# Kernel tuning notes

Hardware: AMD Instinct MI355X
Metric: run time of the kernel (lower is better)

The kernel has to match this reference:

```python
import jax, jax.numpy as jnp
import numpy as np

B, N, DIM, H, DH = 2, 2048, 256, 8, 32
DIM_INNER = H * DH  # 256


def setup_inputs() -> dict:
    key = jax.random.key(0)
    ks = jax.random.split(key, 8)
    s = DIM ** -0.5  # keep activations / logits in a sane range
    return {
        "x_real": jax.random.normal(ks[0], (B, N, DIM), jnp.float32),
        "x_imag": jax.random.normal(ks[1], (B, N, DIM), jnp.float32),
        "wq_r": jax.random.normal(ks[2], (DIM, DIM_INNER), jnp.float32) * s,
        "wq_i": jax.random.normal(ks[3], (DIM, DIM_INNER), jnp.float32) * s,
        "wkv_r": jax.random.normal(ks[4], (DIM, 2 * DIM_INNER), jnp.float32) * s,
        "wkv_i": jax.random.normal(ks[5], (DIM, 2 * DIM_INNER), jnp.float32) * s,
        "wo_r": jax.random.normal(ks[6], (DIM_INNER, DIM), jnp.float32) * s,
        "wo_i": jax.random.normal(ks[7], (DIM_INNER, DIM), jnp.float32) * s,
    }


def _clin(xr, xi, wr, wi):
    # complex linear: (xr + i xi) @ (wr + i wi)
    return xr @ wr - xi @ wi, xr @ wi + xi @ wr


def _split_heads(t):
    b, n, _ = t.shape
    return t.reshape(b, n, H, DH).transpose(0, 2, 1, 3)  # b h n d


def _merge_heads(t):
    b, h, n, d = t.shape
    return t.transpose(0, 2, 1, 3).reshape(b, n, h * d)


def reference(x_real, x_imag, wq_r, wq_i, wkv_r, wkv_i, wo_r, wo_i):
    # complex projections
    qr, qi = _clin(x_real, x_imag, wq_r, wq_i)
    kvr, kvi = _clin(x_real, x_imag, wkv_r, wkv_i)
    kr, vr = jnp.split(kvr, 2, axis=-1)
    ki, vi = jnp.split(kvi, 2, axis=-1)
    qr, qi, kr, ki, vr, vi = map(_split_heads, (qr, qi, kr, ki, vr, vi))

    # complex_attention_complete (sec 3.2 eq 3): 4 real SDPA replicas.
    # q repeat '(c r b)' -> blocks [qr, qr, qi, qi]; k repeat '(r c b)' -> [kr, ki, kr, ki]
    scale = DH ** -0.5
    Q = jnp.stack([qr, qr, qi, qi])        # [4, b, h, n, d]
    K = jnp.stack([kr, ki, kr, ki])
    sim = jnp.einsum('rbhid,rbhjd->rbhij', Q, K) * scale
    A = jax.nn.softmax(sim, axis=-1)       # [4, b, h, n, n]

    av = lambda a, v: jnp.einsum('bhij,bhjd->bhid', a, v)
    # sign-recombine trick: indices [0,3,5,6 | 1,2,4,7], sign [[1,-1,-1,-1],[1,1,1,-1]]
    o_r = av(A[0], vr) - av(A[1], vi) - av(A[2], vi) - av(A[3], vr)
    o_i = av(A[0], vi) + av(A[1], vr) + av(A[2], vr) - av(A[3], vi)

    mr, mi = _merge_heads(o_r), _merge_heads(o_i)
    out_r, out_i = _clin(mr, mi, wo_r, wo_i)
    # real view of the complex output: [b, n, dim, 2]
    return jnp.stack([out_r, out_i], axis=-1)
```

## Files before the change

### kernel.cpp

```cpp
#include <hip/hip_runtime.h>
#include <hip/hip_bf16.h>
#include <math.h>

namespace {
constexpr int kB = 2, kN = 2048, kDim = 256, kH = 8, kDH = 32;
constexpr int kBH = kB * kH;
constexpr long kPlane = (long)kBH * kN * kDH;
constexpr float kQScaleL2 = 0.25506852552f;
}

typedef unsigned short u16;
typedef short short8 __attribute__((ext_vector_type(8)));
typedef short short4v __attribute__((ext_vector_type(4)));
typedef float floatx16 __attribute__((ext_vector_type(16)));
#define MFMA_BF16(a, b, c) __builtin_amdgcn_mfma_f32_32x32x16_bf16(a, b, c, 0, 0, 0)

__device__ inline u16 bf16b(float x) {
    union { float f; unsigned u; } c; c.f = x;
    unsigned r = c.u + 0x7FFFu + ((c.u >> 16) & 1u);
    return (u16)(r >> 16);
}
__device__ inline unsigned pack2(float x, float y) {
    return (unsigned)bf16b(x) | ((unsigned)bf16b(y) << 16);
}
__device__ inline unsigned packtr(float lo, float hi) {
    return __builtin_amdgcn_perm(__float_as_uint(hi), __float_as_uint(lo), 0x07060302u);
}
__device__ inline short8 mk8(const float* e) {
    union { unsigned u[4]; short8 s; } c;
    c.u[0] = packtr(e[0], e[1]);
    c.u[1] = packtr(e[2], e[3]);
    c.u[2] = packtr(e[4], e[5]);
    c.u[3] = packtr(e[6], e[7]);
    return c.s;
}

__global__ __launch_bounds__(256, 2) void prep_w(
    const float* __restrict__ wq_r, const float* __restrict__ wq_i,
    const float* __restrict__ wkv_r, const float* __restrict__ wkv_i,
    const float* __restrict__ wo_r, const float* __restrict__ wo_i,
    u16* __restrict__ Wbig, u16* __restrict__ WoT)
{
    const long base = ((long)blockIdx.x * 256 + threadIdx.x) * 4;
    if (base < 786432) {
        const int c = (int)(base >> 9);
        const int k = (int)(base & 511);
        const int g = c >> 8, d = c & 255;
        const bool hi = k >= 256;
        const int k2 = hi ? k - 256 : k;
        const float* src;
        float sgn = 1.f;
        int col, stride;
        if (g < 2) {
            stride = 256; col = d;
            if (g == 0) { src = hi ? wq_i : wq_r; if (hi) sgn = -1.f; }
            else        { src = hi ? wq_r : wq_i; }
            sgn *= kQScaleL2;
        } else {
            stride = 512;
            col = (g >= 4) ? d + 256 : d;
            if ((g & 1) == 0) { src = hi ? wkv_i : wkv_r; if (hi) sgn = -1.f; }
            else              { src = hi ? wkv_r : wkv_i; }
        }
        short4v v;
        #pragma unroll
        for (int j = 0; j < 4; ++j)
            v[j] = (short)bf16b(src[(long)(k2 + j) * stride + col] * sgn);
        *(short4v*)(Wbig + base) = v;
    } else {
        const long o = base - 786432;
        const int c = (int)(o >> 9);
        const int k = (int)(o & 511);
        const bool hi = k >= 256;
        const int k2 = hi ? k - 256 : k;
        const float* src;
        float sgn = 1.f;
        int col;
        if (c < 256) { col = c;       src = hi ? wo_i : wo_r; if (hi) sgn = -1.f; }
        else         { col = c - 256; src = hi ? wo_r : wo_i; }
        short4v v;
        #pragma unroll
        for (int j = 0; j < 4; ++j)
            v[j] = (short)bf16b(src[(long)(k2 + j) * 256 + col] * sgn);
        *(short4v*)(WoT + o) = v;
    }
}

__global__ __launch_bounds__(256, 2) void gemm_proj(
    const float* __restrict__ xr_g, const float* __restrict__ xi_g,
    const u16* __restrict__ BT,
    u16* __restrict__ qr, u16* __restrict__ qi, u16* __restrict__ kr,
    u16* __restrict__ ki, u16* __restrict__ vrT, u16* __restrict__ viT)
{
    __shared__ __align__(16) u16 sA[128 * 32];
    __shared__ __align__(16) u16 sB[128 * 32];
    const int tid = threadIdx.x;
    const int lane = tid & 63, l31 = lane & 31, lh = lane >> 5;
    const int w = tid >> 6, wrow = w & 1, wcol = w >> 1;
    const int srow = tid >> 2, sseg = tid & 3;
    const int n0 = blockIdx.x * 128, m0 = blockIdx.y * 128;

    floatx16 a00 = {0}, a01 = {0}, a10 = {0}, a11 = {0};

    for (int kt = 0; kt < 512; kt += 32) {
        __syncthreads();
        const float* xbase = (kt < 256) ? xr_g : xi_g;
        const int kc = (kt & 255) + sseg * 8;
        #pragma unroll
        for (int i = 0; i < 2; ++i) {
            const int r = srow + i * 64;
            {
                const float* src = xbase + (long)(m0 + r) * 256 + kc;
                const float4 f0 = *(const float4*)(src);
                const float4 f1 = *(const float4*)(src + 4);
                union { __hip_bfloat162 b[4]; short8 s; } cv;
                cv.b[0] = __float22bfloat162_rn(make_float2(f0.x, f0.y));
                cv.b[1] = __float22bfloat162_rn(make_float2(f0.z, f0.w));
                cv.b[2] = __float22bfloat162_rn(make_float2(f1.x, f1.y));
                cv.b[3] = __float22bfloat162_rn(make_float2(f1.z, f1.w));
                *(short8*)(sA + r * 32 + sseg * 8) = cv.s;
            }
            *(short8*)(sB + r * 32 + sseg * 8) =
                *(const short8*)(BT + (long)(n0 + r) * 512 + kt + sseg * 8);
        }
        __syncthreads();
        #pragma unroll
        for (int s = 0; s < 2; ++s) {
            const int ko = s * 16 + lh * 8;
            const short8 fa0 = *(const short8*)(sA + (wrow * 64 + l31) * 32 + ko);
            const short8 fa1 = *(const short8*)(sA + (wrow * 64 + 32 + l31) * 32 + ko);
            const short8 fb0 = *(const short8*)(sB + (wcol * 64 + l31) * 32 + ko);
            const short8 fb1 = *(const short8*)(sB + (wcol * 64 + 32 + l31) * 32 + ko);
            a00 = MFMA_BF16(fa0, fb0, a00);
            a01 = MFMA_BF16(fa0, fb1, a01);
            a10 = MFMA_BF16(fa1, fb0, a10);
            a11 = MFMA_BF16(fa1, fb1, a11);
        }
    }

    floatx16 accs[2][2] = {{a00, a01}, {a10, a11}};
    #pragma unroll
    for (int rt = 0; rt < 2; ++rt) {
        #pragma unroll
        for (int ct = 0; ct < 2; ++ct) {
            const int colb = n0 + wcol * 64 + ct * 32;
            const int g = colb >> 8;
            const int h = (colb & 255) >> 5;
            if (g < 4) {
                u16* pl = (g == 0) ? qr : (g == 1) ? qi : (g == 2) ? kr : ki;
                #pragma unroll
                for (int reg = 0; reg < 16; ++reg) {
                    const int row = m0 + wrow * 64 + rt * 32 + (reg & 3) + 8 * (reg >> 2) + 4 * lh;
                    const int b = row >> 11, nn = row & 2047;
                    pl[(((long)(b * 8 + h)) * 2048 + nn) * 32 + l31] = bf16b(accs[rt][ct][reg]);
                }
            } else {
                u16* pl = (g == 4) ? vrT : viT;
                #pragma unroll
                for (int reg = 0; reg < 16; ++reg) {
                    const int row = m0 + wrow * 64 + rt * 32 + (reg & 3) + 8 * (reg >> 2) + 4 * lh;
                    const int b = row >> 11, nn = row & 2047;
                    const int np = (nn & ~12) | ((nn & 4) << 1) | ((nn & 8) >> 1);
                    pl[(((long)(b * 8 + h)) * 32 + l31) * 2048 + np] = bf16b(accs[rt][ct][reg]);
                }
            }
        }
    }
}

__global__ __launch_bounds__(512, 2) void attn_kernel(
    const u16* __restrict__ qr_g, const u16* __restrict__ qi_g,
    const u16* __restrict__ kr_g, const u16* __restrict__ ki_g,
    const u16* __restrict__ vrT_g, const u16* __restrict__ viT_g,
    u16* __restrict__ xo)
{
    __shared__ __align__(16) u16 smem[2][2][2][64 * 40];

    const int tid = threadIdx.x;
    const int lane = tid & 63, l31 = lane & 31, lh = lane >> 5;
    const int w = tid >> 6;
    const int strip = w & 1, qtype = (w >> 1) & 1, jhalf = w >> 2;
    const int bh = blockIdx.x;
    const int i0 = blockIdx.y * 64;
    const long base = (long)bh * kN * kDH;

    const u16* qg = (qtype ? qi_g : qr_g) + base;
    short8 qB0, qB1;
    {
        const u16* qp = qg + (long)(i0 + strip * 32 + l31) * kDH;
        qB0 = *(const short8*)(qp + lh * 8);
        qB1 = *(const short8*)(qp + 16 + lh * 8);
    }

    const int t256 = tid & 255;
    const int srow = t256 & 63;
    const int sseg = t256 >> 6;
    const int t0 = jhalf * 32;
    const u16* kptr = ((srow < 32) ? kr_g : ki_g) + base
                    + ((long)t0 * 32 + (srow & 31)) * kDH + sseg * 8;
    const u16* vptr = ((srow < 32) ? vrT_g : viT_g)
                    + ((long)bh * 32 + (srow & 31)) * kN + (long)t0 * 32 + sseg * 8;

    short8 kreg = *(const short8*)kptr;
    short8 vreg = *(const short8*)vptr;

    floatx16 U0r = {0}, U0i = {0}, U1r = {0}, U1i = {0};
    float la0a = 0.f, la0b = 0.f, la1a = 0.f, la1b = 0.f;

    for (int tt = 0; tt < 32; ++tt) {
        u16* bK = smem[jhalf][0][tt & 1];
        u16* bV = smem[jhalf][1][tt & 1];
        *(short8*)(bK + srow * 40 + sseg * 8) = kreg;
        *(short8*)(bV + srow * 40 + sseg * 8) = vreg;
        __syncthreads();
        if (tt < 31) {
            kreg = *(const short8*)(kptr + (long)(tt + 1) * 1024);
            vreg = *(const short8*)(vptr + (tt + 1) * 32);
        }

        const short8 ka0 = *(const short8*)(bK + l31 * 40 + lh * 8);
        const short8 ka1 = *(const short8*)(bK + l31 * 40 + 16 + lh * 8);
        const short8 kb0 = *(const short8*)(bK + (32 + l31) * 40 + lh * 8);
        const short8 kb1 = *(const short8*)(bK + (32 + l31) * 40 + 16 + lh * 8);
        floatx16 S0 = {0}, S1 = {0};
        S0 = MFMA_BF16(ka0, qB0, S0);
        S0 = MFMA_BF16(ka1, qB1, S0);
        S1 = MFMA_BF16(kb0, qB0, S1);
        S1 = MFMA_BF16(kb1, qB1, S1);

        float e0[16], e1[16];
        #pragma unroll
        for (int r = 0; r < 16; ++r) {
            e0[r] = __builtin_amdgcn_exp2f(S0[r]);
            if (r & 1) la0a += e0[r]; else la0b += e0[r];
        }
        #pragma unroll
        for (int r = 0; r < 16; ++r) {
            e1[r] = __builtin_amdgcn_exp2f(S1[r]);
            if (r & 1) la1a += e1[r]; else la1b += e1[r];
        }
        const short8 F0a = mk8(&e0[0]);
        const short8 F0b = mk8(&e0[8]);
        const short8 F1a = mk8(&e1[0]);
        const short8 F1b = mk8(&e1[8]);

        const short8 va0 = *(const short8*)(bV + l31 * 40 + lh * 8);
        const short8 va1 = *(const short8*)(bV + l31 * 40 + 16 + lh * 8);
        const short8 vb0 = *(const short8*)(bV + (32 + l31) * 40 + lh * 8);
        const short8 vb1 = *(const short8*)(bV + (32 + l31) * 40 + 16 + lh * 8);

        U0r = MFMA_BF16(va0, F0a, U0r);
        U0r = MFMA_BF16(va1, F0b, U0r);
        U0i = MFMA_BF16(vb0, F0a, U0i);
        U0i = MFMA_BF16(vb1, F0b, U0i);
        U1r = MFMA_BF16(va0, F1a, U1r);
        U1r = MFMA_BF16(va1, F1b, U1r);
        U1i = MFMA_BF16(vb0, F1a, U1i);
        U1i = MFMA_BF16(vb1, F1b, U1i);
    }

    float La0 = la0a + la0b;
    float La1 = la1a + la1b;
    La0 += __shfl_xor(La0, 32);
    La1 += __shfl_xor(La1, 32);

    __syncthreads();
    float* sLa = (float*)smem;
    float* sPo = (float*)((u16*)smem + 2048);
    sLa[(w * 2 + 0) * 64 + lane] = La0;
    sLa[(w * 2 + 1) * 64 + lane] = La1;
    __syncthreads();
    const int pw = w ^ 4;
    const float iL0 = 1.f / (La0 + sLa[(pw * 2 + 0) * 64 + lane]);
    const float iL1 = 1.f / (La1 + sLa[(pw * 2 + 1) * 64 + lane]);

    float po_r[16], po_i[16];
    #pragma unroll
    for (int r = 0; r < 16; ++r) {
        if (qtype == 0) {
            po_r[r] =  U0r[r] * iL0 - U1i[r] * iL1;
            po_i[r] =  U0i[r] * iL0 + U1r[r] * iL1;
        } else {
            po_r[r] = -U0i[r] * iL0 - U1r[r] * iL1;
            po_i[r] =  U0r[r] * iL0 - U1i[r] * iL1;
        }
    }

    if (jhalf == 1) {
        float* dst = sPo + ((size_t)(w - 4) * 64 + lane) * 33;
        #pragma unroll
        for (int g = 0; g < 4; ++g) {
            *(float4*)(dst + 4 * g) =
                make_float4(po_r[4 * g], po_r[4 * g + 1], po_r[4 * g + 2], po_r[4 * g + 3]);
            *(float4*)(dst + 16 + 4 * g) =
                make_float4(po_i[4 * g], po_i[4 * g + 1], po_i[4 * g + 2], po_i[4 * g + 3]);
        }
    }
    __syncthreads();
    if (jhalf == 0) {
        const float* src = sPo + ((size_t)w * 64 + lane) * 33;
        #pragma unroll
        for (int g = 0; g < 4; ++g) {
            const float4 ar = *(const float4*)(src + 4 * g);
            const float4 ai = *(const float4*)(src + 16 + 4 * g);
            po_r[4 * g + 0] += ar.x; po_r[4 * g + 1] += ar.y;
            po_r[4 * g + 2] += ar.z; po_r[4 * g + 3] += ar.w;
            po_i[4 * g + 0] += ai.x; po_i[4 * g + 1] += ai.y;
            po_i[4 * g + 2] += ai.z; po_i[4 * g + 3] += ai.w;
        }
    }
    __syncthreads();
    if (jhalf == 0 && qtype == 1) {
        float* dst = sPo + ((size_t)(w - 2) * 64 + lane) * 33;
        #pragma unroll
        for (int g = 0; g < 4; ++g) {
            *(float4*)(dst + 4 * g) =
                make_float4(po_r[4 * g], po_r[4 * g + 1], po_r[4 * g + 2], po_r[4 * g + 3]);
            *(float4*)(dst + 16 + 4 * g) =
                make_float4(po_i[4 * g], po_i[4 * g + 1], po_i[4 * g + 2], po_i[4 * g + 3]);
        }
    }
    __syncthreads();
    if (w < 2) {
        const float* src = sPo + ((size_t)w * 64 + lane) * 33;
        #pragma unroll
        for (int g = 0; g < 4; ++g) {
            const float4 ar = *(const float4*)(src + 4 * g);
            const float4 ai = *(const float4*)(src + 16 + 4 * g);
            po_r[4 * g + 0] += ar.x; po_r[4 * g + 1] += ar.y;
            po_r[4 * g + 2] += ar.z; po_r[4 * g + 3] += ar.w;
            po_i[4 * g + 0] += ai.x; po_i[4 * g + 1] += ai.y;
            po_i[4 * g + 2] += ai.z; po_i[4 * g + 3] += ai.w;
        }
        const int b = bh >> 3, h = bh & 7;
        u16* xrow = xo + ((long)(b * 2048) + i0 + strip * 32 + l31) * 512 + h * 32;
        #pragma unroll
        for (int g = 0; g < 4; ++g) {
            const int d0 = 8 * g + 4 * lh;
            union { unsigned u[2]; uint2 v; } pr, pi;
            pr.u[0] = pack2(po_r[4 * g + 0], po_r[4 * g + 1]);
            pr.u[1] = pack2(po_r[4 * g + 2], po_r[4 * g + 3]);
            pi.u[0] = pack2(po_i[4 * g + 0], po_i[4 * g + 1]);
            pi.u[1] = pack2(po_i[4 * g + 2], po_i[4 * g + 3]);
            *(uint2*)(xrow + d0) = pr.v;
            *(uint2*)(xrow + 256 + d0) = pi.v;
        }
    }
}

__global__ __launch_bounds__(256, 2) void gemm_oproj(
    const u16* __restrict__ Xo, const u16* __restrict__ BT, float* __restrict__ out)
{
    __shared__ __align__(16) u16 sA[128 * 32];
    __shared__ __align__(16) u16 sB[128 * 32];
    const int tid = threadIdx.x;
    const int lane = tid & 63, l31 = lane & 31, lh = lane >> 5;
    const int w = tid >> 6, wrow = w & 1, wcol = w >> 1;
    const int srow = tid >> 2, sseg = tid & 3;
    const int n0 = blockIdx.x * 128, m0 = blockIdx.y * 128;

    floatx16 a00 = {0}, a01 = {0}, a10 = {0}, a11 = {0};

    for (int kt = 0; kt < 512; kt += 32) {
        __syncthreads();
        #pragma unroll
        for (int i = 0; i < 2; ++i) {
            const int r = srow + i * 64;
            *(short8*)(sA + r * 32 + sseg * 8) =
                *(const short8*)(Xo + (long)(m0 + r) * 512 + kt + sseg * 8);
            *(short8*)(sB + r * 32 + sseg * 8) =
                *(const short8*)(BT + (long)(n0 + r) * 512 + kt + sseg * 8);
        }
        __syncthreads();
        #pragma unroll
        for (int s = 0; s < 2; ++s) {
            const int ko = s * 16 + lh * 8;
            const short8 fa0 = *(const short8*)(sA + (wrow * 64 + l31) * 32 + ko);
            const short8 fa1 = *(const short8*)(sA + (wrow * 64 + 32 + l31) * 32 + ko);
            const short8 fb0 = *(const short8*)(sB + (wcol * 64 + l31) * 32 + ko);
            const short8 fb1 = *(const short8*)(sB + (wcol * 64 + 32 + l31) * 32 + ko);
            a00 = MFMA_BF16(fa0, fb0, a00);
            a01 = MFMA_BF16(fa0, fb1, a01);
            a10 = MFMA_BF16(fa1, fb0, a10);
            a11 = MFMA_BF16(fa1, fb1, a11);
        }
    }

    floatx16 accs[2][2] = {{a00, a01}, {a10, a11}};
    #pragma unroll
    for (int rt = 0; rt < 2; ++rt) {
        #pragma unroll
        for (int ct = 0; ct < 2; ++ct) {
            const int colb = n0 + wcol * 64 + ct * 32;
            #pragma unroll
            for (int reg = 0; reg < 16; ++reg) {
                const int row = m0 + wrow * 64 + rt * 32 + (reg & 3) + 8 * (reg >> 2) + 4 * lh;
                const int col = colb + l31;
                const float val = accs[rt][ct][reg];
                if (colb < 256) out[(long)row * 512 + col * 2] = val;
                else            out[(long)row * 512 + (col - 256) * 2 + 1] = val;
            }
        }
    }
}

extern "C" void kernel_launch(void* const* d_in, const int* in_sizes, int n_in,
                              void* d_out, int out_size, void* d_ws, size_t ws_size,
                              hipStream_t stream) {
    const float* xr    = (const float*)d_in[0];
    const float* xi    = (const float*)d_in[1];
    const float* wq_r  = (const float*)d_in[2];
    const float* wq_i  = (const float*)d_in[3];
    const float* wkv_r = (const float*)d_in[4];
    const float* wkv_i = (const float*)d_in[5];
    const float* wo_r  = (const float*)d_in[6];
    const float* wo_i  = (const float*)d_in[7];
    float* out = (float*)d_out;

    u16* ws16 = (u16*)d_ws;
    u16* qr   = ws16 + 0 * kPlane;
    u16* qi   = ws16 + 1 * kPlane;
    u16* kr   = ws16 + 2 * kPlane;
    u16* ki   = ws16 + 3 * kPlane;
    u16* vrT  = ws16 + 4 * kPlane;
    u16* viT  = ws16 + 5 * kPlane;
    u16* xo   = ws16 + 6 * kPlane;
    u16* Wbig = ws16 + 8 * kPlane;
    u16* WoT  = Wbig + 786432;

    prep_w<<<1024, 256, 0, stream>>>(wq_r, wq_i, wkv_r, wkv_i, wo_r, wo_i, Wbig, WoT);
    gemm_proj<<<dim3(12, 32), 256, 0, stream>>>(xr, xi, Wbig, qr, qi, kr, ki, vrT, viT);
    attn_kernel<<<dim3(kBH, kN / 64), 512, 0, stream>>>(qr, qi, kr, ki, vrT, viT, xo);
    gemm_oproj<<<dim3(4, 32), 256, 0, stream>>>(xo, WoT, out);
}
```

Before: 177.8 us.

## Split attention warps by key type instead of key-sequence half

Warps were each assigned half of the key sequence and computed both the real and imaginary key-score tiles. Now each warp covers the whole key sequence for a single key type (real or imaginary). That halves the per-iteration MFMA and exp work per warp, doubles the iteration count, and removes the cross-warp softmax-denominator exchange. A single shared double buffer now holds K and V for all warps, loaded by all 512 threads. The trade-off is twice as many barrier-synchronised iterations, each doing less work, which may expose more load and sync latency.

```diff
diff --git a/kernel.cpp b/kernel.cpp
--- a/kernel.cpp
+++ b/kernel.cpp
@@ -174,12 +174,13 @@
     const u16* __restrict__ vrT_g, const u16* __restrict__ viT_g,
     u16* __restrict__ xo)
 {
-    __shared__ __align__(16) u16 smem[2][2][2][64 * 40];
+    __shared__ __align__(16) unsigned char smem[33792];
+    u16* base16 = (u16*)smem;
 
     const int tid = threadIdx.x;
     const int lane = tid & 63, l31 = lane & 31, lh = lane >> 5;
     const int w = tid >> 6;
-    const int strip = w & 1, qtype = (w >> 1) & 1, jhalf = w >> 2;
+    const int strip = w & 1, qtype = (w >> 1) & 1, ktype = w >> 2;
     const int bh = blockIdx.x;
     const int i0 = blockIdx.y * 64;
     const long base = (long)bh * kN * kDH;
@@ -192,101 +193,83 @@
         qB1 = *(const short8*)(qp + 16 + lh * 8);
     }
 
-    const int t256 = tid & 255;
-    const int srow = t256 & 63;
-    const int sseg = t256 >> 6;
-    const int t0 = jhalf * 32;
-    const u16* kptr = ((srow < 32) ? kr_g : ki_g) + base
-                    + ((long)t0 * 32 + (srow & 31)) * kDH + sseg * 8;
-    const u16* vptr = ((srow < 32) ? vrT_g : viT_g)
-                    + ((long)bh * 32 + (srow & 31)) * kN + (long)t0 * 32 + sseg * 8;
-
-    short8 kreg = *(const short8*)kptr;
-    short8 vreg = *(const short8*)vptr;
-
-    floatx16 U0r = {0}, U0i = {0}, U1r = {0}, U1i = {0};
-    float la0a = 0.f, la0b = 0.f, la1a = 0.f, la1b = 0.f;
-
-    for (int tt = 0; tt < 32; ++tt) {
-        u16* bK = smem[jhalf][0][tt & 1];
-        u16* bV = smem[jhalf][1][tt & 1];
-        *(short8*)(bK + srow * 40 + sseg * 8) = kreg;
-        *(short8*)(bV + srow * 40 + sseg * 8) = vreg;
+    const int kv = tid >> 8;
+    const int srow = (tid >> 2) & 63;
+    const int sseg = tid & 3;
+    const int soff = kv * 2560 + srow * 40 + sseg * 8;
+    const u16* sptr;
+    long sstride;
+    if (kv == 0) {
+        sptr = ((srow < 32) ? kr_g : ki_g) + base + (long)(srow & 31) * kDH + sseg * 8;
+        sstride = 1024;
+    } else {
+        sptr = ((srow < 32) ? vrT_g : viT_g)
+             + ((long)bh * 32 + (srow & 31)) * kN + sseg * 8;
+        sstride = 32;
+    }
+    short8 sreg = *(const short8*)sptr;
+
+    floatx16 Uvr = {0}, Uvi = {0};
+    float laa = 0.f, lab = 0.f;
+
+    for (int tt = 0; tt < 64; ++tt) {
+        u16* buf = base16 + (tt & 1) * 5120;
+        *(short8*)(buf + soff) = sreg;
         __syncthreads();
-        if (tt < 31) {
-            kreg = *(const short8*)(kptr + (long)(tt + 1) * 1024);
-            vreg = *(const short8*)(vptr + (tt + 1) * 32);
-        }
-
-        const short8 ka0 = *(const short8*)(bK + l31 * 40 + lh * 8);
-        const short8 ka1 = *(const short8*)(bK + l31 * 40 + 16 + lh * 8);
-        const short8 kb0 = *(const short8*)(bK + (32 + l31) * 40 + lh * 8);
-        const short8 kb1 = *(const short8*)(bK + (32 + l31) * 40 + 16 + lh * 8);
-        floatx16 S0 = {0}, S1 = {0};
-        S0 = MFMA_BF16(ka0, qB0, S0);
-        S0 = MFMA_BF16(ka1, qB1, S0);
-        S1 = MFMA_BF16(kb0, qB0, S1);
-        S1 = MFMA_BF16(kb1, qB1, S1);
-
-        float e0[16], e1[16];
+        if (tt < 63) sreg = *(const short8*)(sptr + (long)(tt + 1) * sstride);
+
+        u16* bK = buf;
+        u16* bV = buf + 2560;
+
+        const u16* krow = bK + (ktype * 32 + l31) * 40 + lh * 8;
+        const short8 ka0 = *(const short8*)(krow);
+        const short8 ka1 = *(const short8*)(krow + 16);
+        floatx16 S = {0};
+        S = MFMA_BF16(ka0, qB0, S);
+        S = MFMA_BF16(ka1, qB1, S);
+
+        float e[16];
         #pragma unroll
         for (int r = 0; r < 16; ++r) {
-            e0[r] = __builtin_amdgcn_exp2f(S0[r]);
-            if (r & 1) la0a += e0[r]; else la0b += e0[r];
-        }
-        #pragma unroll
-        for (int r = 0; r < 16; ++r) {
-            e1[r] = __builtin_amdgcn_exp2f(S1[r]);
-            if (r & 1) la1a += e1[r]; else la1b += e1[r];
-        }
-        const short8 F0a = mk8(&e0[0]);
-        const short8 F0b = mk8(&e0[8]);
-        const short8 F1a = mk8(&e1[0]);
-        const short8 F1b = mk8(&e1[8]);
+            e[r] = __builtin_amdgcn_exp2f(S[r]);
+            if (r & 1) laa += e[r]; else lab += e[r];
+        }
+        const short8 Fa = mk8(&e[0]);
+        const short8 Fb = mk8(&e[8]);
 
         const short8 va0 = *(const short8*)(bV + l31 * 40 + lh * 8);
         const short8 va1 = *(const short8*)(bV + l31 * 40 + 16 + lh * 8);
         const short8 vb0 = *(const short8*)(bV + (32 + l31) * 40 + lh * 8);
         const short8 vb1 = *(const short8*)(bV + (32 + l31) * 40 + 16 + lh * 8);
 
-        U0r = MFMA_BF16(va0, F0a, U0r);
-        U0r = MFMA_BF16(va1, F0b, U0r);
-        U0i = MFMA_BF16(vb0, F0a, U0i);
-        U0i = MFMA_BF16(vb1, F0b, U0i);
-        U1r = MFMA_BF16(va0, F1a, U1r);
-        U1r = MFMA_BF16(va1, F1b, U1r);
-        U1i = MFMA_BF16(vb0, F1a, U1i);
-        U1i = MFMA_BF16(vb1, F1b, U1i);
-    }
-
-    float La0 = la0a + la0b;
-    float La1 = la1a + la1b;
-    La0 += __shfl_xor(La0, 32);
-    La1 += __shfl_xor(La1, 32);
-
-    __syncthreads();
-    float* sLa = (float*)smem;
-    float* sPo = (float*)((u16*)smem + 2048);
-    sLa[(w * 2 + 0) * 64 + lane] = La0;
-    sLa[(w * 2 + 1) * 64 + lane] = La1;
-    __syncthreads();
-    const int pw = w ^ 4;
-    const float iL0 = 1.f / (La0 + sLa[(pw * 2 + 0) * 64 + lane]);
-    const float iL1 = 1.f / (La1 + sLa[(pw * 2 + 1) * 64 + lane]);
+        Uvr = MFMA_BF16(va0, Fa, Uvr);
+        Uvr = MFMA_BF16(va1, Fb, Uvr);
+        Uvi = MFMA_BF16(vb0, Fa, Uvi);
+        Uvi = MFMA_BF16(vb1, Fb, Uvi);
+    }
+
+    float La = laa + lab;
+    La += __shfl_xor(La, 32);
+    const float iL = 1.f / La;
 
     float po_r[16], po_i[16];
     #pragma unroll
     for (int r = 0; r < 16; ++r) {
-        if (qtype == 0) {
-            po_r[r] =  U0r[r] * iL0 - U1i[r] * iL1;
-            po_i[r] =  U0i[r] * iL0 + U1r[r] * iL1;
+        const float ur = Uvr[r] * iL, ui = Uvi[r] * iL;
+        if (qtype == ktype) {
+            const float s = qtype ? -1.f : 1.f;
+            po_r[r] = s * ur;
+            po_i[r] = s * ui;
         } else {
-            po_r[r] = -U0i[r] * iL0 - U1r[r] * iL1;
-            po_i[r] =  U0r[r] * iL0 - U1i[r] * iL1;
-        }
-    }
-
-    if (jhalf == 1) {
+            po_r[r] = -ui;
+            po_i[r] =  ur;
+        }
+    }
+
+    __syncthreads();
+    float* sPo = (float*)smem;
+
+    if (ktype == 1) {
         float* dst = sPo + ((size_t)(w - 4) * 64 + lane) * 33;
         #pragma unroll
         for (int g = 0; g < 4; ++g) {
@@ -297,7 +280,7 @@
         }
     }
     __syncthreads();
-    if (jhalf == 0) {
+    if (ktype == 0) {
         const float* src = sPo + ((size_t)w * 64 + lane) * 33;
         #pragma unroll
         for (int g = 0; g < 4; ++g) {
@@ -310,7 +293,7 @@
         }
     }
     __syncthreads();
-    if (jhalf == 0 && qtype == 1) {
+    if (ktype == 0 && qtype == 1) {
         float* dst = sPo + ((size_t)(w - 2) * 64 + lane) * 33;
         #pragma unroll
         for (int g = 0; g < 4; ++g) {
```

Measured after the change: 177.3 us. Within noise of the previous version (-0.3%).
